# Optimization experiments

Hardware: AMD Instinct MI355X
Metric: run time of the kernel (lower is better)

## Reference

```python
import jax, jax.numpy as jnp
import numpy as np

B, T = 256, 64          # batch, rollout length
D, S, A, E, H = 1024, 64, 32, 1024, 1024  # deter, stoch, action, obs_embed, hidden


def setup_inputs() -> dict:
    key = jax.random.key(0)
    ks = jax.random.split(key, 12)
    f32 = jnp.float32

    def w(k, shape, fan_in):
        return (jax.random.normal(k, shape, f32) / np.float32(np.sqrt(fan_in)))

    return dict(
        obs_embeds=jax.random.normal(ks[0], (B, T, E), f32),
        action_embs=jax.random.normal(ks[1], (B, T, A), f32),
        noise_prior=jax.random.normal(ks[2], (T - 1, B, S), f32),  # randn_like in prior
        noise_post=jax.random.normal(ks[3], (T - 1, B, S), f32),   # randn_like in posterior
        # fc_state_action_embed: Linear(S+A -> D)
        W_sa=w(ks[4], (D, S + A), S + A), b_sa=jnp.zeros((D,), f32),
        # GRUCell(D, D): torch layout [3D, D] with gate order r, z, n
        W_ih=w(ks[5], (3 * D, D), D), b_ih=jnp.zeros((3 * D,), f32),
        W_hh=w(ks[6], (3 * D, D), D), b_hh=jnp.zeros((3 * D,), f32),
        # state_prior: Linear(D->H), ELU, Linear(H->2S)
        Wp1=w(ks[7], (H, D), D), bp1=jnp.zeros((H,), f32),
        Wp2=w(ks[8], (2 * S, H), H), bp2=jnp.zeros((2 * S,), f32),
        # state_posterior: Linear(D+E->H), ELU, Linear(H->2S)
        Wq1=w(ks[9], (H, D + E), D + E), bq1=jnp.zeros((H,), f32),
        Wq2=w(ks[10], (2 * S, H), H), bq2=jnp.zeros((2 * S,), f32),
    )


def reference(obs_embeds, action_embs, noise_prior, noise_post,
              W_sa, b_sa, W_ih, b_ih, W_hh, b_hh,
              Wp1, bp1, Wp2, bp2, Wq1, bq1, Wq2, bq2):
    # observe_rollout: init state is zeros; step t uses obs[:, t+1], action[:, t].
    b = obs_embeds.shape[0]
    h0 = jnp.zeros((b, D), obs_embeds.dtype)
    s0 = jnp.zeros((b, S), obs_embeds.dtype)
    obs_seq = jnp.swapaxes(obs_embeds[:, 1:], 0, 1)   # [T-1, B, E]
    act_seq = jnp.swapaxes(action_embs[:, :-1], 0, 1)  # [T-1, B, A]

    def step(carry, xs):
        h, s = carry  # posterior deter / stoch state from previous step
        obs, act, ep, eq = xs
        # prior: embed (stoch, action) -> GRU update
        e = jax.nn.elu(jnp.concatenate([s, act], -1) @ W_sa.T + b_sa)
        gi = e @ W_ih.T + b_ih
        gh = h @ W_hh.T + b_hh
        ir, iz, ia = jnp.split(gi, 3, axis=-1)
        hr, hz, ha = jnp.split(gh, 3, axis=-1)
        r = jax.nn.sigmoid(ir + hr)
        z = jax.nn.sigmoid(iz + hz)
        n = jnp.tanh(ia + r * ha)
        h_new = (1.0 - z) * n + z * h  # prior deter state
        # prior dist + reparam sample
        pm = jax.nn.elu(h_new @ Wp1.T + bp1) @ Wp2.T + bp2
        pmean, pstd = jnp.split(pm, 2, axis=-1)
        pstd = jax.nn.softplus(pstd) + 0.1
        pstoch = pmean + pstd * ep
        # posterior dist + reparam sample (conditioned on h_new and obs)
        qm = jax.nn.elu(jnp.concatenate([h_new, obs], -1) @ Wq1.T + bq1) @ Wq2.T + bq2
        qmean, qstd = jnp.split(qm, 2, axis=-1)
        qstd = jax.nn.softplus(qstd) + 0.1
        qstoch = qmean + qstd * eq
        out = jnp.concatenate([h_new, pmean, pstd, pstoch, qmean, qstd, qstoch], -1)
        return (h_new, qstoch), out

    _, outs = jax.lax.scan(step, (h0, s0), (obs_seq, act_seq, noise_prior, noise_post))
    # outs: [T-1, B, D + 6S] = (prior deter, prior mean/std/stoch, post mean/std/stoch)
    return outs
```

## Files before the change

kernel.cpp:

```cpp
#include <hip/hip_runtime.h>

typedef __attribute__((ext_vector_type(8))) short short8;
typedef __attribute__((ext_vector_type(4))) float f32x4;

#define OSTEP (256*1408)

#define OFF_WIH  ((size_t)0)
#define OFF_WHH  ((size_t)3145728)
#define OFF_WP1  ((size_t)6291456)
#define OFF_WQ1  ((size_t)7340032)
#define OFF_WP2  ((size_t)9437184)
#define OFF_WQ2  ((size_t)9568256)
#define OFF_HBF0 ((size_t)9699328)
#define OFF_HBF1 ((size_t)9961472)
#define OFF_EBF  ((size_t)10223616)
#define OFF_P1E  ((size_t)10485760)
#define OFF_Q1E  ((size_t)10747904)
#define F32_BYTE_OFF ((size_t)22020096)

__device__ __forceinline__ unsigned short f2bf(float f){
  union { float f; unsigned u; } v; v.f = f;
  unsigned u = v.u;
  u += 0x7fffu + ((u >> 16) & 1u);
  return (unsigned short)(u >> 16);
}
__device__ __forceinline__ float sigf(float x){ return 1.0f/(1.0f+__expf(-x)); }
__device__ __forceinline__ float tanhf_(float x){
  float e = __expf(-2.0f*fabsf(x));
  float t = (1.0f-e)/(1.0f+e);
  return x>=0.f ? t : -t;
}
__device__ __forceinline__ float eluf(float x){ return x>0.f ? x : __expf(x)-1.0f; }
__device__ __forceinline__ float softplusf(float x){ return x>20.f ? x : log1pf(__expf(x)); }
__device__ __forceinline__ short8 ld8(const unsigned short* p){ return *(const short8*)p; }

__global__ void k_prep(const float* __restrict__ wih, const float* __restrict__ whh,
                       const float* __restrict__ wp1, const float* __restrict__ wq1,
                       const float* __restrict__ wp2, const float* __restrict__ wq2,
                       unsigned short* __restrict__ dst){
  size_t i4 = ((size_t)blockIdx.x*256 + threadIdx.x)*4;
  const size_t total = 9699328;
  if(i4 >= total) return;
  const float* src; size_t off;
  if(i4 < 3145728){ src=wih; off=0; }
  else if(i4 < 6291456){ src=whh; off=3145728; }
  else if(i4 < 7340032){ src=wp1; off=6291456; }
  else if(i4 < 9437184){ src=wq1; off=7340032; }
  else if(i4 < 9568256){ src=wp2; off=9437184; }
  else { src=wq2; off=9568256; }
  size_t j = i4 - off;
  float4 v = *(const float4*)(src + j);
  unsigned long long p = (unsigned long long)f2bf(v.x)
                       | ((unsigned long long)f2bf(v.y) << 16)
                       | ((unsigned long long)f2bf(v.z) << 32)
                       | ((unsigned long long)f2bf(v.w) << 48);
  *(unsigned long long*)(dst + i4) = p;
}

__global__ __launch_bounds__(384) void k_gru(
    const unsigned short* __restrict__ e_bf,
    const unsigned short* __restrict__ h_bf,
    const unsigned short* __restrict__ wih_bf,
    const unsigned short* __restrict__ whh_bf,
    const float* __restrict__ b_ih, const float* __restrict__ b_hh,
    const float* __restrict__ hprev, int hprev_ld,
    float* __restrict__ out_t,
    unsigned short* __restrict__ hnext_bf)
{
  int bx = blockIdx.x, by = blockIdx.y;
  int tid = threadIdx.x, w = tid >> 6, lane = tid & 63;
  int g = w % 3; bool isI = (w < 3);
  const unsigned short* A  = isI ? e_bf  : h_bf;
  const unsigned short* Bw = isI ? wih_bf : whh_bf;
  int brow = g*1024 + bx*32;
  int arow = by*32;
  int l15 = lane & 15, q8 = (lane >> 4)*8;

  f32x4 z4 = {0.f,0.f,0.f,0.f};
  f32x4 acc00=z4, acc01=z4, acc10=z4, acc11=z4;

  const unsigned short* pa0 = A  + (size_t)(arow + l15)*1024 + q8;
  const unsigned short* pa1 = pa0 + 16*1024;
  const unsigned short* pb0 = Bw + (size_t)(brow + l15)*1024 + q8;
  const unsigned short* pb1 = pb0 + 16*1024;

  #pragma unroll 4
  for(int kk=0; kk<1024; kk+=32){
    short8 a0 = ld8(pa0+kk), a1 = ld8(pa1+kk);
    short8 b0 = ld8(pb0+kk), b1 = ld8(pb1+kk);
    acc00 = __builtin_amdgcn_mfma_f32_16x16x32_bf16(a0,b0,acc00,0,0,0);
    acc01 = __builtin_amdgcn_mfma_f32_16x16x32_bf16(a0,b1,acc01,0,0,0);
    acc10 = __builtin_amdgcn_mfma_f32_16x16x32_bf16(a1,b0,acc10,0,0,0);
    acc11 = __builtin_amdgcn_mfma_f32_16x16x32_bf16(a1,b1,acc11,0,0,0);
  }

  __shared__ float sg[6][32][33];
  int rr = (lane>>4)*4;
  #pragma unroll
  for(int v=0; v<4; v++){
    sg[w][0 +rr+v][0 +l15] = acc00[v];
    sg[w][0 +rr+v][16+l15] = acc01[v];
    sg[w][16+rr+v][0 +l15] = acc10[v];
    sg[w][16+rr+v][16+l15] = acc11[v];
  }
  __syncthreads();

  for(int i=tid; i<1024; i+=384){
    int m = i>>5, n = i&31;
    int d = bx*32+n, b = by*32+m;
    float ir = sg[0][m][n] + b_ih[d];
    float iz = sg[1][m][n] + b_ih[1024+d];
    float ia = sg[2][m][n] + b_ih[2048+d];
    float hr = sg[3][m][n] + b_hh[d];
    float hz = sg[4][m][n] + b_hh[1024+d];
    float ha = sg[5][m][n] + b_hh[2048+d];
    float r = sigf(ir+hr), zz = sigf(iz+hz);
    float nn = tanhf_(ia + r*ha);
    float hold = hprev[(size_t)b*hprev_ld + d];
    float hnew = (1.f-zz)*nn + zz*hold;
    out_t[(size_t)b*1408 + d] = hnew;
    hnext_bf[(size_t)b*1024 + d] = f2bf(hnew);
  }
}

__global__ __launch_bounds__(256) void k_heads1(
    const unsigned short* __restrict__ hnew_bf,
    const float* __restrict__ obs, int tcol,
    const unsigned short* __restrict__ wp1_bf,
    const unsigned short* __restrict__ wq1_bf,
    const float* __restrict__ bp1, const float* __restrict__ bq1,
    unsigned short* __restrict__ p1e, unsigned short* __restrict__ q1e)
{
  int bx = blockIdx.x, by = blockIdx.y;
  bool isQ = (bx >= 32); int nt = bx & 31;
  int tid = threadIdx.x, w = tid>>6, lane = tid&63;
  int mi = w & 1, ni = w >> 1;
  int l15 = lane & 15, q8 = (lane>>4)*8;
  int arowg = by*32 + mi*16 + l15;
  int browg = nt*32 + ni*16 + l15;

  f32x4 acc = {0.f,0.f,0.f,0.f};
  const unsigned short* pa = hnew_bf + (size_t)arowg*1024 + q8;

  if(!isQ){
    const unsigned short* pb = wp1_bf + (size_t)browg*1024 + q8;
    #pragma unroll 4
    for(int kk=0; kk<1024; kk+=32){
      acc = __builtin_amdgcn_mfma_f32_16x16x32_bf16(ld8(pa+kk), ld8(pb+kk), acc,0,0,0);
    }
  } else {
    const unsigned short* pb = wq1_bf + (size_t)browg*2048 + q8;
    #pragma unroll 4
    for(int kk=0; kk<1024; kk+=32){
      acc = __builtin_amdgcn_mfma_f32_16x16x32_bf16(ld8(pa+kk), ld8(pb+kk), acc,0,0,0);
    }
    const float* obsrow = obs + ((size_t)arowg*64 + tcol)*1024 + q8;
    #pragma unroll 4
    for(int kk=0; kk<1024; kk+=32){
      const float4* f = (const float4*)(obsrow + kk);
      float4 x0 = f[0], x1 = f[1];
      short8 a;
      a[0]=(short)f2bf(x0.x); a[1]=(short)f2bf(x0.y); a[2]=(short)f2bf(x0.z); a[3]=(short)f2bf(x0.w);
      a[4]=(short)f2bf(x1.x); a[5]=(short)f2bf(x1.y); a[6]=(short)f2bf(x1.z); a[7]=(short)f2bf(x1.w);
      acc = __builtin_amdgcn_mfma_f32_16x16x32_bf16(a, ld8(pb+1024+kk), acc,0,0,0);
    }
  }

  const float* bias = isQ ? bq1 : bp1;
  unsigned short* dst = isQ ? q1e : p1e;
  int col = browg;
  float bv = bias[col];
  #pragma unroll
  for(int v=0; v<4; v++){
    int b = by*32 + mi*16 + (lane>>4)*4 + v;
    float val = eluf(acc[v] + bv);
    dst[(size_t)b*1024 + col] = f2bf(val);
  }
}

__global__ __launch_bounds__(256) void k_heads2(
    const unsigned short* __restrict__ p1e, const unsigned short* __restrict__ q1e,
    const unsigned short* __restrict__ wp2_bf, const unsigned short* __restrict__ wq2_bf,
    const float* __restrict__ bp2, const float* __restrict__ bq2,
    float* __restrict__ pm, float* __restrict__ qm)
{
  int bx = blockIdx.x, by = blockIdx.y;
  int col0 = bx*32; bool isQ = (col0 >= 128); int c0 = col0 & 127;
  int tid = threadIdx.x, w = tid>>6, lane = tid&63;
  int mi = w & 1, ni = w >> 1;
  int l15 = lane & 15, q8 = (lane>>4)*8;
  const unsigned short* A  = isQ ? q1e : p1e;
  const unsigned short* Bw = isQ ? wq2_bf : wp2_bf;
  const float* bias = isQ ? bq2 : bp2;
  float* outb = isQ ? qm : pm;

  int arowg = by*32 + mi*16 + l15;
  int browg = c0 + ni*16 + l15;
  f32x4 acc = {0.f,0.f,0.f,0.f};
  const unsigned short* pa = A  + (size_t)arowg*1024 + q8;
  const unsigned short* pb = Bw + (size_t)browg*1024 + q8;
  #pragma unroll 4
  for(int kk=0; kk<1024; kk+=32){
    acc = __builtin_amdgcn_mfma_f32_16x16x32_bf16(ld8(pa+kk), ld8(pb+kk), acc,0,0,0);
  }
  float bv = bias[browg];
  #pragma unroll
  for(int v=0; v<4; v++){
    int b = by*32 + mi*16 + (lane>>4)*4 + v;
    outb[(size_t)b*128 + browg] = acc[v] + bv;
  }
}

__global__ __launch_bounds__(256) void k_sample_e(
    int t_out, int t_act,
    const float* __restrict__ pm, const float* __restrict__ qm,
    const float* __restrict__ noise_p, const float* __restrict__ noise_q,
    const float* __restrict__ act, const float* __restrict__ w_sa,
    const float* __restrict__ b_sa,
    float* __restrict__ out, unsigned short* __restrict__ e_bf)
{
  __shared__ float qst[32*64];
  __shared__ float sact[32*32];
  int bx = blockIdx.x, by = blockIdx.y, tid = threadIdx.x;

  if(t_out >= 0){
    float* out_t = out + (size_t)t_out*OSTEP;
    for(int i=tid; i<2048; i+=256){
      int m = i>>6, s = i&63; int b = by*32+m;
      float qmean = qm[(size_t)b*128 + s];
      float qstd  = softplusf(qm[(size_t)b*128 + 64 + s]) + 0.1f;
      float qs = qmean + qstd * noise_q[((size_t)t_out*256 + b)*64 + s];
      qst[m*64+s] = qs;
      if(bx == 0){
        float pmean = pm[(size_t)b*128 + s];
        float pstd  = softplusf(pm[(size_t)b*128 + 64 + s]) + 0.1f;
        float ps = pmean + pstd * noise_p[((size_t)t_out*256 + b)*64 + s];
        float* o = out_t + (size_t)b*1408;
        o[1024+s] = pmean; o[1088+s] = pstd; o[1152+s] = ps;
        o[1216+s] = qmean; o[1280+s] = qstd; o[1344+s] = qs;
      }
    }
  } else {
    for(int i=tid; i<2048; i+=256) qst[i] = 0.f;
  }
  for(int i=tid; i<1024; i+=256){
    int m = i>>5, k = i&31;
    sact[i] = act[((size_t)(by*32+m)*64 + t_act)*32 + k];
  }
  __syncthreads();

  int n = tid & 31, mb = tid >> 5;
  int d = bx*32 + n;
  const float* wrow = w_sa + (size_t)d*96;
  float a0=b_sa[d], a1=a0, a2=a0, a3=a0;
  for(int k=0; k<64; k++){
    float wv = wrow[k];
    a0 += qst[(mb+ 0)*64+k]*wv;
    a1 += qst[(mb+ 8)*64+k]*wv;
    a2 += qst[(mb+16)*64+k]*wv;
    a3 += qst[(mb+24)*64+k]*wv;
  }
  for(int k=0; k<32; k++){
    float wv = wrow[64+k];
    a0 += sact[(mb+ 0)*32+k]*wv;
    a1 += sact[(mb+ 8)*32+k]*wv;
    a2 += sact[(mb+16)*32+k]*wv;
    a3 += sact[(mb+24)*32+k]*wv;
  }
  e_bf[(size_t)(by*32+mb+ 0)*1024 + d] = f2bf(eluf(a0));
  e_bf[(size_t)(by*32+mb+ 8)*1024 + d] = f2bf(eluf(a1));
  e_bf[(size_t)(by*32+mb+16)*1024 + d] = f2bf(eluf(a2));
  e_bf[(size_t)(by*32+mb+24)*1024 + d] = f2bf(eluf(a3));
}

extern "C" void kernel_launch(void* const* d_in, const int* in_sizes, int n_in,
                              void* d_out, int out_size, void* d_ws, size_t ws_size,
                              hipStream_t stream) {
  const float* obs = (const float*)d_in[0];
  const float* act = (const float*)d_in[1];
  const float* np_ = (const float*)d_in[2];
  const float* nq_ = (const float*)d_in[3];
  const float* wsa = (const float*)d_in[4];
  const float* bsa = (const float*)d_in[5];
  const float* wih = (const float*)d_in[6];
  const float* bih = (const float*)d_in[7];
  const float* whh = (const float*)d_in[8];
  const float* bhh = (const float*)d_in[9];
  const float* wp1 = (const float*)d_in[10];
  const float* bp1 = (const float*)d_in[11];
  const float* wp2 = (const float*)d_in[12];
  const float* bp2 = (const float*)d_in[13];
  const float* wq1 = (const float*)d_in[14];
  const float* bq1 = (const float*)d_in[15];
  const float* wq2 = (const float*)d_in[16];
  const float* bq2 = (const float*)d_in[17];
  float* out = (float*)d_out;

  unsigned short* wsb = (unsigned short*)d_ws;
  unsigned short* wihb = wsb + OFF_WIH;
  unsigned short* whhb = wsb + OFF_WHH;
  unsigned short* wp1b = wsb + OFF_WP1;
  unsigned short* wq1b = wsb + OFF_WQ1;
  unsigned short* wp2b = wsb + OFF_WP2;
  unsigned short* wq2b = wsb + OFF_WQ2;
  unsigned short* hbf0 = wsb + OFF_HBF0;
  unsigned short* hbf1 = wsb + OFF_HBF1;
  unsigned short* ebf  = wsb + OFF_EBF;
  unsigned short* p1e  = wsb + OFF_P1E;
  unsigned short* q1e  = wsb + OFF_Q1E;
  float* f32b = (float*)((char*)d_ws + F32_BYTE_OFF);
  float* h0 = f32b;
  float* pm = f32b + 262144;
  float* qm = f32b + 262144 + 32768;

  hipMemsetAsync(hbf0, 0, 262144*2, stream);
  hipMemsetAsync(h0, 0, 262144*4, stream);

  k_prep<<<9472, 256, 0, stream>>>(wih, whh, wp1, wq1, wp2, wq2, wsb);

  k_sample_e<<<dim3(32,8), 256, 0, stream>>>(-1, 0, pm, qm, np_, nq_, act, wsa, bsa, out, ebf);

  for(int t=0; t<63; t++){
    const unsigned short* hb = (t&1) ? hbf1 : hbf0;
    unsigned short* hbn      = (t&1) ? hbf0 : hbf1;
    const float* hprev = t ? (out + (size_t)(t-1)*OSTEP) : h0;
    int hld = t ? 1408 : 1024;
    k_gru<<<dim3(32,8), 384, 0, stream>>>(ebf, hb, wihb, whhb, bih, bhh,
                                          hprev, hld, out + (size_t)t*OSTEP, hbn);
    k_heads1<<<dim3(64,8), 256, 0, stream>>>(hbn, obs, t+1, wp1b, wq1b, bp1, bq1, p1e, q1e);
    k_heads2<<<dim3(8,8), 256, 0, stream>>>(p1e, q1e, wp2b, wq2b, bp2, bq2, pm, qm);
    k_sample_e<<<dim3(32,8), 256, 0, stream>>>(t, t+1, pm, qm, np_, nq_, act, wsa, bsa, out, ebf);
  }
}
```

Measured before the change: 5.976 ms.

## Halve batch tile per block and split-K head GEMMs to raise parallelism

The GRU kernel now handles 16 batch rows per block instead of 32, doubling the grid to 512 blocks. The two head kernels likewise use 16-row tiles, and their four waves are split across two K halves, reduced through shared memory before bias and activation. The goal is to fill more of the MI355X compute units in these small per-step GEMMs, which run under a long serial chain of launches. The cost is that each weight tile is read by twice as many blocks, adding L2 traffic, plus an extra LDS reduction and barrier in the head kernels.

```diff
diff --git a/kernel.cpp b/kernel.cpp
--- a/kernel.cpp
+++ b/kernel.cpp
@@ -2,6 +2,7 @@
 
 typedef __attribute__((ext_vector_type(8))) short short8;
 typedef __attribute__((ext_vector_type(4))) float f32x4;
+typedef unsigned short us;
 
 #define OSTEP (256*1408)
 
@@ -32,12 +33,12 @@
 }
 __device__ __forceinline__ float eluf(float x){ return x>0.f ? x : __expf(x)-1.0f; }
 __device__ __forceinline__ float softplusf(float x){ return x>20.f ? x : log1pf(__expf(x)); }
-__device__ __forceinline__ short8 ld8(const unsigned short* p){ return *(const short8*)p; }
+__device__ __forceinline__ short8 ld8(const us* p){ return *(const short8*)p; }
 
 __global__ void k_prep(const float* __restrict__ wih, const float* __restrict__ whh,
                        const float* __restrict__ wp1, const float* __restrict__ wq1,
                        const float* __restrict__ wp2, const float* __restrict__ wq2,
-                       unsigned short* __restrict__ dst){
+                       us* __restrict__ dst){
   size_t i4 = ((size_t)blockIdx.x*256 + threadIdx.x)*4;
   const size_t total = 9699328;
   if(i4 >= total) return;
@@ -58,56 +59,48 @@
 }
 
 __global__ __launch_bounds__(384) void k_gru(
-    const unsigned short* __restrict__ e_bf,
-    const unsigned short* __restrict__ h_bf,
-    const unsigned short* __restrict__ wih_bf,
-    const unsigned short* __restrict__ whh_bf,
+    const us* __restrict__ e_bf, const us* __restrict__ h_bf,
+    const us* __restrict__ wih_bf, const us* __restrict__ whh_bf,
     const float* __restrict__ b_ih, const float* __restrict__ b_hh,
     const float* __restrict__ hprev, int hprev_ld,
-    float* __restrict__ out_t,
-    unsigned short* __restrict__ hnext_bf)
+    float* __restrict__ out_t, us* __restrict__ hnext_bf)
 {
   int bx = blockIdx.x, by = blockIdx.y;
   int tid = threadIdx.x, w = tid >> 6, lane = tid & 63;
   int g = w % 3; bool isI = (w < 3);
-  const unsigned short* A  = isI ? e_bf  : h_bf;
-  const unsigned short* Bw = isI ? wih_bf : whh_bf;
+  const us* A  = isI ? e_bf  : h_bf;
+  const us* Bw = isI ? wih_bf : whh_bf;
   int brow = g*1024 + bx*32;
-  int arow = by*32;
+  int arow = by*16;
   int l15 = lane & 15, q8 = (lane >> 4)*8;
 
   f32x4 z4 = {0.f,0.f,0.f,0.f};
-  f32x4 acc00=z4, acc01=z4, acc10=z4, acc11=z4;
-
-  const unsigned short* pa0 = A  + (size_t)(arow + l15)*1024 + q8;
-  const unsigned short* pa1 = pa0 + 16*1024;
-  const unsigned short* pb0 = Bw + (size_t)(brow + l15)*1024 + q8;
-  const unsigned short* pb1 = pb0 + 16*1024;
-
-  #pragma unroll 4
+  f32x4 acc0=z4, acc1=z4;
+
+  const us* pa0 = A  + (size_t)(arow + l15)*1024 + q8;
+  const us* pb0 = Bw + (size_t)(brow + l15)*1024 + q8;
+  const us* pb1 = pb0 + 16*1024;
+
+  #pragma unroll 8
   for(int kk=0; kk<1024; kk+=32){
-    short8 a0 = ld8(pa0+kk), a1 = ld8(pa1+kk);
+    short8 a0 = ld8(pa0+kk);
     short8 b0 = ld8(pb0+kk), b1 = ld8(pb1+kk);
-    acc00 = __builtin_amdgcn_mfma_f32_16x16x32_bf16(a0,b0,acc00,0,0,0);
-    acc01 = __builtin_amdgcn_mfma_f32_16x16x32_bf16(a0,b1,acc01,0,0,0);
-    acc10 = __builtin_amdgcn_mfma_f32_16x16x32_bf16(a1,b0,acc10,0,0,0);
-    acc11 = __builtin_amdgcn_mfma_f32_16x16x32_bf16(a1,b1,acc11,0,0,0);
-  }
-
-  __shared__ float sg[6][32][33];
+    acc0 = __builtin_amdgcn_mfma_f32_16x16x32_bf16(a0,b0,acc0,0,0,0);
+    acc1 = __builtin_amdgcn_mfma_f32_16x16x32_bf16(a0,b1,acc1,0,0,0);
+  }
+
+  __shared__ float sg[6][16][33];
   int rr = (lane>>4)*4;
   #pragma unroll
   for(int v=0; v<4; v++){
-    sg[w][0 +rr+v][0 +l15] = acc00[v];
-    sg[w][0 +rr+v][16+l15] = acc01[v];
-    sg[w][16+rr+v][0 +l15] = acc10[v];
-    sg[w][16+rr+v][16+l15] = acc11[v];
+    sg[w][rr+v][0 +l15] = acc0[v];
+    sg[w][rr+v][16+l15] = acc1[v];
   }
   __syncthreads();
 
-  for(int i=tid; i<1024; i+=384){
+  for(int i=tid; i<512; i+=384){
     int m = i>>5, n = i&31;
-    int d = bx*32+n, b = by*32+m;
+    int d = bx*32+n, b = by*16+m;
     float ir = sg[0][m][n] + b_ih[d];
     float iz = sg[1][m][n] + b_ih[1024+d];
     float ia = sg[2][m][n] + b_ih[2048+d];
@@ -124,90 +117,107 @@
 }
 
 __global__ __launch_bounds__(256) void k_heads1(
-    const unsigned short* __restrict__ hnew_bf,
+    const us* __restrict__ hnew_bf,
     const float* __restrict__ obs, int tcol,
-    const unsigned short* __restrict__ wp1_bf,
-    const unsigned short* __restrict__ wq1_bf,
+    const us* __restrict__ wp1_bf, const us* __restrict__ wq1_bf,
     const float* __restrict__ bp1, const float* __restrict__ bq1,
-    unsigned short* __restrict__ p1e, unsigned short* __restrict__ q1e)
+    us* __restrict__ p1e, us* __restrict__ q1e)
 {
   int bx = blockIdx.x, by = blockIdx.y;
   bool isQ = (bx >= 32); int nt = bx & 31;
   int tid = threadIdx.x, w = tid>>6, lane = tid&63;
-  int mi = w & 1, ni = w >> 1;
+  int ni = w & 1, kh = w >> 1;
   int l15 = lane & 15, q8 = (lane>>4)*8;
-  int arowg = by*32 + mi*16 + l15;
+  int arowg = by*16 + l15;
   int browg = nt*32 + ni*16 + l15;
+  int k0 = kh*512;
 
   f32x4 acc = {0.f,0.f,0.f,0.f};
-  const unsigned short* pa = hnew_bf + (size_t)arowg*1024 + q8;
+  const us* pa = hnew_bf + (size_t)arowg*1024 + q8 + k0;
 
   if(!isQ){
-    const unsigned short* pb = wp1_bf + (size_t)browg*1024 + q8;
-    #pragma unroll 4
-    for(int kk=0; kk<1024; kk+=32){
+    const us* pb = wp1_bf + (size_t)browg*1024 + q8 + k0;
+    #pragma unroll 8
+    for(int kk=0; kk<512; kk+=32){
       acc = __builtin_amdgcn_mfma_f32_16x16x32_bf16(ld8(pa+kk), ld8(pb+kk), acc,0,0,0);
     }
   } else {
-    const unsigned short* pb = wq1_bf + (size_t)browg*2048 + q8;
-    #pragma unroll 4
-    for(int kk=0; kk<1024; kk+=32){
+    const us* pb = wq1_bf + (size_t)browg*2048 + q8 + k0;
+    #pragma unroll 8
+    for(int kk=0; kk<512; kk+=32){
       acc = __builtin_amdgcn_mfma_f32_16x16x32_bf16(ld8(pa+kk), ld8(pb+kk), acc,0,0,0);
     }
-    const float* obsrow = obs + ((size_t)arowg*64 + tcol)*1024 + q8;
+    const float* obsrow = obs + ((size_t)arowg*64 + tcol)*1024 + q8 + k0;
+    const us* pb2 = wq1_bf + (size_t)browg*2048 + 1024 + q8 + k0;
     #pragma unroll 4
-    for(int kk=0; kk<1024; kk+=32){
+    for(int kk=0; kk<512; kk+=32){
       const float4* f = (const float4*)(obsrow + kk);
       float4 x0 = f[0], x1 = f[1];
       short8 a;
       a[0]=(short)f2bf(x0.x); a[1]=(short)f2bf(x0.y); a[2]=(short)f2bf(x0.z); a[3]=(short)f2bf(x0.w);
       a[4]=(short)f2bf(x1.x); a[5]=(short)f2bf(x1.y); a[6]=(short)f2bf(x1.z); a[7]=(short)f2bf(x1.w);
-      acc = __builtin_amdgcn_mfma_f32_16x16x32_bf16(a, ld8(pb+1024+kk), acc,0,0,0);
+      acc = __builtin_amdgcn_mfma_f32_16x16x32_bf16(a, ld8(pb2+kk), acc,0,0,0);
     }
   }
 
+  __shared__ float sg[4][16][17];
+  int rr=(lane>>4)*4;
+  #pragma unroll
+  for(int v=0;v<4;v++) sg[w][rr+v][l15] = acc[v];
+  __syncthreads();
+
   const float* bias = isQ ? bq1 : bp1;
-  unsigned short* dst = isQ ? q1e : p1e;
-  int col = browg;
-  float bv = bias[col];
-  #pragma unroll
-  for(int v=0; v<4; v++){
-    int b = by*32 + mi*16 + (lane>>4)*4 + v;
-    float val = eluf(acc[v] + bv);
-    dst[(size_t)b*1024 + col] = f2bf(val);
+  us* dst = isQ ? q1e : p1e;
+  for(int i=tid; i<512; i+=256){
+    int m = i>>5, n = i&31;
+    int nni = n>>4, nn = n&15;
+    float val = sg[nni][m][nn] + sg[2+nni][m][nn];
+    int col = nt*32 + n;
+    int b = by*16 + m;
+    dst[(size_t)b*1024 + col] = f2bf(eluf(val + bias[col]));
   }
 }
 
 __global__ __launch_bounds__(256) void k_heads2(
-    const unsigned short* __restrict__ p1e, const unsigned short* __restrict__ q1e,
-    const unsigned short* __restrict__ wp2_bf, const unsigned short* __restrict__ wq2_bf,
+    const us* __restrict__ p1e, const us* __restrict__ q1e,
+    const us* __restrict__ wp2_bf, const us* __restrict__ wq2_bf,
     const float* __restrict__ bp2, const float* __restrict__ bq2,
     float* __restrict__ pm, float* __restrict__ qm)
 {
   int bx = blockIdx.x, by = blockIdx.y;
   int col0 = bx*32; bool isQ = (col0 >= 128); int c0 = col0 & 127;
   int tid = threadIdx.x, w = tid>>6, lane = tid&63;
-  int mi = w & 1, ni = w >> 1;
+  int ni = w & 1, kh = w >> 1;
   int l15 = lane & 15, q8 = (lane>>4)*8;
-  const unsigned short* A  = isQ ? q1e : p1e;
-  const unsigned short* Bw = isQ ? wq2_bf : wp2_bf;
+  const us* A  = isQ ? q1e : p1e;
+  const us* Bw = isQ ? wq2_bf : wp2_bf;
   const float* bias = isQ ? bq2 : bp2;
   float* outb = isQ ? qm : pm;
 
-  int arowg = by*32 + mi*16 + l15;
+  int arowg = by*16 + l15;
   int browg = c0 + ni*16 + l15;
+  int k0 = kh*512;
   f32x4 acc = {0.f,0.f,0.f,0.f};
-  const unsigned short* pa = A  + (size_t)arowg*1024 + q8;
-  const unsigned short* pb = Bw + (size_t)browg*1024 + q8;
-  #pragma unroll 4
-  for(int kk=0; kk<1024; kk+=32){
+  const us* pa = A  + (size_t)arowg*1024 + q8 + k0;
+  const us* pb = Bw + (size_t)browg*1024 + q8 + k0;
+  #pragma unroll 8
+  for(int kk=0; kk<512; kk+=32){
     acc = __builtin_amdgcn_mfma_f32_16x16x32_bf16(ld8(pa+kk), ld8(pb+kk), acc,0,0,0);
   }
-  float bv = bias[browg];
+
+  __shared__ float sg[4][16][17];
+  int rr=(lane>>4)*4;
   #pragma unroll
-  for(int v=0; v<4; v++){
-    int b = by*32 + mi*16 + (lane>>4)*4 + v;
-    outb[(size_t)b*128 + browg] = acc[v] + bv;
+  for(int v=0;v<4;v++) sg[w][rr+v][l15] = acc[v];
+  __syncthreads();
+
+  for(int i=tid; i<512; i+=256){
+    int m = i>>5, n = i&31;
+    int nni = n>>4, nn = n&15;
+    float val = sg[nni][m][nn] + sg[2+nni][m][nn];
+    int col = c0 + n;
+    int b = by*16 + m;
+    outb[(size_t)b*128 + col] = val + bias[col];
   }
 }
 
@@ -217,7 +227,7 @@
     const float* __restrict__ noise_p, const float* __restrict__ noise_q,
     const float* __restrict__ act, const float* __restrict__ w_sa,
     const float* __restrict__ b_sa,
-    float* __restrict__ out, unsigned short* __restrict__ e_bf)
+    float* __restrict__ out, us* __restrict__ e_bf)
 {
   __shared__ float qst[32*64];
   __shared__ float sact[32*32];
@@ -295,19 +305,19 @@
   const float* wq2 = (const float*)d_in[16];
   const float* bq2 = (const float*)d_in[17];
   float* out = (float*)d_out;
-
-  unsigned short* wsb = (unsigned short*)d_ws;
-  unsigned short* wihb = wsb + OFF_WIH;
-  unsigned short* whhb = wsb + OFF_WHH;
-  unsigned short* wp1b = wsb + OFF_WP1;
-  unsigned short* wq1b = wsb + OFF_WQ1;
-  unsigned short* wp2b = wsb + OFF_WP2;
-  unsigned short* wq2b = wsb + OFF_WQ2;
-  unsigned short* hbf0 = wsb + OFF_HBF0;
-  unsigned short* hbf1 = wsb + OFF_HBF1;
-  unsigned short* ebf  = wsb + OFF_EBF;
-  unsigned short* p1e  = wsb + OFF_P1E;
-  unsigned short* q1e  = wsb + OFF_Q1E;
+  us* wsb = (us*)d_ws;
+
+  us* wihb = wsb + OFF_WIH;
+  us* whhb = wsb + OFF_WHH;
+  us* wp1b = wsb + OFF_WP1;
+  us* wq1b = wsb + OFF_WQ1;
+  us* wp2b = wsb + OFF_WP2;
+  us* wq2b = wsb + OFF_WQ2;
+  us* hbf0 = wsb + OFF_HBF0;
+  us* hbf1 = wsb + OFF_HBF1;
+  us* ebf  = wsb + OFF_EBF;
+  us* p1e  = wsb + OFF_P1E;
+  us* q1e  = wsb + OFF_Q1E;
   float* f32b = (float*)((char*)d_ws + F32_BYTE_OFF);
   float* h0 = f32b;
   float* pm = f32b + 262144;
@@ -321,14 +331,14 @@
   k_sample_e<<<dim3(32,8), 256, 0, stream>>>(-1, 0, pm, qm, np_, nq_, act, wsa, bsa, out, ebf);
 
   for(int t=0; t<63; t++){
-    const unsigned short* hb = (t&1) ? hbf1 : hbf0;
-    unsigned short* hbn      = (t&1) ? hbf0 : hbf1;
+    const us* hb = (t&1) ? hbf1 : hbf0;
+    us* hbn      = (t&1) ? hbf0 : hbf1;
     const float* hprev = t ? (out + (size_t)(t-1)*OSTEP) : h0;
     int hld = t ? 1408 : 1024;
-    k_gru<<<dim3(32,8), 384, 0, stream>>>(ebf, hb, wihb, whhb, bih, bhh,
-                                          hprev, hld, out + (size_t)t*OSTEP, hbn);
-    k_heads1<<<dim3(64,8), 256, 0, stream>>>(hbn, obs, t+1, wp1b, wq1b, bp1, bq1, p1e, q1e);
-    k_heads2<<<dim3(8,8), 256, 0, stream>>>(p1e, q1e, wp2b, wq2b, bp2, bq2, pm, qm);
+    k_gru<<<dim3(32,16), 384, 0, stream>>>(ebf, hb, wihb, whhb, bih, bhh,
+                                           hprev, hld, out + (size_t)t*OSTEP, hbn);
+    k_heads1<<<dim3(64,16), 256, 0, stream>>>(hbn, obs, t+1, wp1b, wq1b, bp1, bq1, p1e, q1e);
+    k_heads2<<<dim3(8,16), 256, 0, stream>>>(p1e, q1e, wp2b, wq2b, bp2, bq2, pm, qm);
     k_sample_e<<<dim3(32,8), 256, 0, stream>>>(t, t+1, pm, qm, np_, nq_, act, wsa, bsa, out, ebf);
   }
 }
```

Result: slower. 6.226 ms (+4.2%).

## Fuse second head layer into sampling kernel and stage obs in LDS

Applied to the files above, without the earlier changes.

Merges the head output GEMM into the sampling/embedding kernel so pm/qm stay in shared memory, cutting one launch and a global round-trip per step. Each block now recomputes the full 256-wide head output for its rows, which is redundant across column blocks, and the grid shrinks to 64 blocks with more work per thread. The posterior head kernel also converts the obs rows to bf16 once into LDS instead of per warp.

```diff
diff --git a/kernel.cpp b/kernel.cpp
--- a/kernel.cpp
+++ b/kernel.cpp
@@ -2,6 +2,7 @@
 
 typedef __attribute__((ext_vector_type(8))) short short8;
 typedef __attribute__((ext_vector_type(4))) float f32x4;
+typedef unsigned short us;
 
 #define OSTEP (256*1408)
 
@@ -32,12 +33,12 @@
 }
 __device__ __forceinline__ float eluf(float x){ return x>0.f ? x : __expf(x)-1.0f; }
 __device__ __forceinline__ float softplusf(float x){ return x>20.f ? x : log1pf(__expf(x)); }
-__device__ __forceinline__ short8 ld8(const unsigned short* p){ return *(const short8*)p; }
+__device__ __forceinline__ short8 ld8(const us* p){ return *(const short8*)p; }
 
 __global__ void k_prep(const float* __restrict__ wih, const float* __restrict__ whh,
                        const float* __restrict__ wp1, const float* __restrict__ wq1,
                        const float* __restrict__ wp2, const float* __restrict__ wq2,
-                       unsigned short* __restrict__ dst){
+                       us* __restrict__ dst){
   size_t i4 = ((size_t)blockIdx.x*256 + threadIdx.x)*4;
   const size_t total = 9699328;
   if(i4 >= total) return;
@@ -58,20 +59,17 @@
 }
 
 __global__ __launch_bounds__(384) void k_gru(
-    const unsigned short* __restrict__ e_bf,
-    const unsigned short* __restrict__ h_bf,
-    const unsigned short* __restrict__ wih_bf,
-    const unsigned short* __restrict__ whh_bf,
+    const us* __restrict__ e_bf, const us* __restrict__ h_bf,
+    const us* __restrict__ wih_bf, const us* __restrict__ whh_bf,
     const float* __restrict__ b_ih, const float* __restrict__ b_hh,
     const float* __restrict__ hprev, int hprev_ld,
-    float* __restrict__ out_t,
-    unsigned short* __restrict__ hnext_bf)
+    float* __restrict__ out_t, us* __restrict__ hnext_bf)
 {
   int bx = blockIdx.x, by = blockIdx.y;
   int tid = threadIdx.x, w = tid >> 6, lane = tid & 63;
   int g = w % 3; bool isI = (w < 3);
-  const unsigned short* A  = isI ? e_bf  : h_bf;
-  const unsigned short* Bw = isI ? wih_bf : whh_bf;
+  const us* A  = isI ? e_bf  : h_bf;
+  const us* Bw = isI ? wih_bf : whh_bf;
   int brow = g*1024 + bx*32;
   int arow = by*32;
   int l15 = lane & 15, q8 = (lane >> 4)*8;
@@ -79,10 +77,10 @@
   f32x4 z4 = {0.f,0.f,0.f,0.f};
   f32x4 acc00=z4, acc01=z4, acc10=z4, acc11=z4;
 
-  const unsigned short* pa0 = A  + (size_t)(arow + l15)*1024 + q8;
-  const unsigned short* pa1 = pa0 + 16*1024;
-  const unsigned short* pb0 = Bw + (size_t)(brow + l15)*1024 + q8;
-  const unsigned short* pb1 = pb0 + 16*1024;
+  const us* pa0 = A  + (size_t)(arow + l15)*1024 + q8;
+  const us* pa1 = pa0 + 16*1024;
+  const us* pb0 = Bw + (size_t)(brow + l15)*1024 + q8;
+  const us* pb1 = pb0 + 16*1024;
 
   #pragma unroll 4
   for(int kk=0; kk<1024; kk+=32){
@@ -124,13 +122,13 @@
 }
 
 __global__ __launch_bounds__(256) void k_heads1(
-    const unsigned short* __restrict__ hnew_bf,
+    const us* __restrict__ hnew_bf,
     const float* __restrict__ obs, int tcol,
-    const unsigned short* __restrict__ wp1_bf,
-    const unsigned short* __restrict__ wq1_bf,
+    const us* __restrict__ wp1_bf, const us* __restrict__ wq1_bf,
     const float* __restrict__ bp1, const float* __restrict__ bq1,
-    unsigned short* __restrict__ p1e, unsigned short* __restrict__ q1e)
+    us* __restrict__ p1e, us* __restrict__ q1e)
 {
+  __shared__ us sobs[32][1032];
   int bx = blockIdx.x, by = blockIdx.y;
   bool isQ = (bx >= 32); int nt = bx & 31;
   int tid = threadIdx.x, w = tid>>6, lane = tid&63;
@@ -140,34 +138,42 @@
   int browg = nt*32 + ni*16 + l15;
 
   f32x4 acc = {0.f,0.f,0.f,0.f};
-  const unsigned short* pa = hnew_bf + (size_t)arowg*1024 + q8;
+  const us* pa = hnew_bf + (size_t)arowg*1024 + q8;
 
   if(!isQ){
-    const unsigned short* pb = wp1_bf + (size_t)browg*1024 + q8;
+    const us* pb = wp1_bf + (size_t)browg*1024 + q8;
     #pragma unroll 4
     for(int kk=0; kk<1024; kk+=32){
       acc = __builtin_amdgcn_mfma_f32_16x16x32_bf16(ld8(pa+kk), ld8(pb+kk), acc,0,0,0);
     }
   } else {
-    const unsigned short* pb = wq1_bf + (size_t)browg*2048 + q8;
+    for(int i=tid; i<32*256; i+=256){
+      int r = i>>8, c4 = (i&255)*4;
+      const float4* f = (const float4*)(obs + ((size_t)(by*32+r)*64 + tcol)*1024 + c4);
+      float4 x = *f;
+      unsigned long long p = (unsigned long long)f2bf(x.x)
+                           | ((unsigned long long)f2bf(x.y) << 16)
+                           | ((unsigned long long)f2bf(x.z) << 32)
+                           | ((unsigned long long)f2bf(x.w) << 48);
+      *(unsigned long long*)(&sobs[r][c4]) = p;
+    }
+    __syncthreads();
+
+    const us* pb = wq1_bf + (size_t)browg*2048 + q8;
     #pragma unroll 4
     for(int kk=0; kk<1024; kk+=32){
       acc = __builtin_amdgcn_mfma_f32_16x16x32_bf16(ld8(pa+kk), ld8(pb+kk), acc,0,0,0);
     }
-    const float* obsrow = obs + ((size_t)arowg*64 + tcol)*1024 + q8;
+    const us* po = &sobs[mi*16 + l15][q8];
+    const us* pb2 = wq1_bf + (size_t)browg*2048 + 1024 + q8;
     #pragma unroll 4
     for(int kk=0; kk<1024; kk+=32){
-      const float4* f = (const float4*)(obsrow + kk);
-      float4 x0 = f[0], x1 = f[1];
-      short8 a;
-      a[0]=(short)f2bf(x0.x); a[1]=(short)f2bf(x0.y); a[2]=(short)f2bf(x0.z); a[3]=(short)f2bf(x0.w);
-      a[4]=(short)f2bf(x1.x); a[5]=(short)f2bf(x1.y); a[6]=(short)f2bf(x1.z); a[7]=(short)f2bf(x1.w);
-      acc = __builtin_amdgcn_mfma_f32_16x16x32_bf16(a, ld8(pb+1024+kk), acc,0,0,0);
+      acc = __builtin_amdgcn_mfma_f32_16x16x32_bf16(ld8(po+kk), ld8(pb2+kk), acc,0,0,0);
     }
   }
 
   const float* bias = isQ ? bq1 : bp1;
-  unsigned short* dst = isQ ? q1e : p1e;
+  us* dst = isQ ? q1e : p1e;
   int col = browg;
   float bv = bias[col];
   #pragma unroll
@@ -178,62 +184,55 @@
   }
 }
 
-__global__ __launch_bounds__(256) void k_heads2(
-    const unsigned short* __restrict__ p1e, const unsigned short* __restrict__ q1e,
-    const unsigned short* __restrict__ wp2_bf, const unsigned short* __restrict__ wq2_bf,
+__global__ __launch_bounds__(256) void k_tail(
+    int t_out, int t_act,
+    const us* __restrict__ p1e, const us* __restrict__ q1e,
+    const us* __restrict__ wp2_bf, const us* __restrict__ wq2_bf,
     const float* __restrict__ bp2, const float* __restrict__ bq2,
-    float* __restrict__ pm, float* __restrict__ qm)
-{
-  int bx = blockIdx.x, by = blockIdx.y;
-  int col0 = bx*32; bool isQ = (col0 >= 128); int c0 = col0 & 127;
-  int tid = threadIdx.x, w = tid>>6, lane = tid&63;
-  int mi = w & 1, ni = w >> 1;
-  int l15 = lane & 15, q8 = (lane>>4)*8;
-  const unsigned short* A  = isQ ? q1e : p1e;
-  const unsigned short* Bw = isQ ? wq2_bf : wp2_bf;
-  const float* bias = isQ ? bq2 : bp2;
-  float* outb = isQ ? qm : pm;
-
-  int arowg = by*32 + mi*16 + l15;
-  int browg = c0 + ni*16 + l15;
-  f32x4 acc = {0.f,0.f,0.f,0.f};
-  const unsigned short* pa = A  + (size_t)arowg*1024 + q8;
-  const unsigned short* pb = Bw + (size_t)browg*1024 + q8;
-  #pragma unroll 4
-  for(int kk=0; kk<1024; kk+=32){
-    acc = __builtin_amdgcn_mfma_f32_16x16x32_bf16(ld8(pa+kk), ld8(pb+kk), acc,0,0,0);
-  }
-  float bv = bias[browg];
-  #pragma unroll
-  for(int v=0; v<4; v++){
-    int b = by*32 + mi*16 + (lane>>4)*4 + v;
-    outb[(size_t)b*128 + browg] = acc[v] + bv;
-  }
-}
-
-__global__ __launch_bounds__(256) void k_sample_e(
-    int t_out, int t_act,
-    const float* __restrict__ pm, const float* __restrict__ qm,
     const float* __restrict__ noise_p, const float* __restrict__ noise_q,
     const float* __restrict__ act, const float* __restrict__ w_sa,
     const float* __restrict__ b_sa,
-    float* __restrict__ out, unsigned short* __restrict__ e_bf)
+    float* __restrict__ out, us* __restrict__ e_bf)
 {
+  __shared__ float pmq[32][258];
   __shared__ float qst[32*64];
   __shared__ float sact[32*32];
   int bx = blockIdx.x, by = blockIdx.y, tid = threadIdx.x;
+  int w = tid>>6, lane = tid&63;
+  int l15 = lane&15, q8 = (lane>>4)*8;
+
+  if(t_out >= 0){
+    int mi = w&1, cg = w>>1;
+    const us* A  = cg ? q1e : p1e;
+    const us* Bw = cg ? wq2_bf : wp2_bf;
+    int arowg = by*32 + mi*16 + l15;
+    const us* pa = A + (size_t)arowg*1024 + q8;
+    for(int ct=0; ct<8; ct++){
+      const us* pb = Bw + (size_t)(ct*16 + l15)*1024 + q8;
+      f32x4 acc = {0.f,0.f,0.f,0.f};
+      #pragma unroll 4
+      for(int kk=0; kk<1024; kk+=32){
+        acc = __builtin_amdgcn_mfma_f32_16x16x32_bf16(ld8(pa+kk), ld8(pb+kk), acc,0,0,0);
+      }
+      int rr = (lane>>4)*4;
+      #pragma unroll
+      for(int v=0; v<4; v++)
+        pmq[mi*16 + rr + v][cg*128 + ct*16 + l15] = acc[v];
+    }
+  }
+  __syncthreads();
 
   if(t_out >= 0){
     float* out_t = out + (size_t)t_out*OSTEP;
     for(int i=tid; i<2048; i+=256){
       int m = i>>6, s = i&63; int b = by*32+m;
-      float qmean = qm[(size_t)b*128 + s];
-      float qstd  = softplusf(qm[(size_t)b*128 + 64 + s]) + 0.1f;
+      float qmean = pmq[m][128+s] + bq2[s];
+      float qstd  = softplusf(pmq[m][192+s] + bq2[64+s]) + 0.1f;
       float qs = qmean + qstd * noise_q[((size_t)t_out*256 + b)*64 + s];
       qst[m*64+s] = qs;
       if(bx == 0){
-        float pmean = pm[(size_t)b*128 + s];
-        float pstd  = softplusf(pm[(size_t)b*128 + 64 + s]) + 0.1f;
+        float pmean = pmq[m][s] + bp2[s];
+        float pstd  = softplusf(pmq[m][64+s] + bp2[64+s]) + 0.1f;
         float ps = pmean + pstd * noise_p[((size_t)t_out*256 + b)*64 + s];
         float* o = out_t + (size_t)b*1408;
         o[1024+s] = pmean; o[1088+s] = pstd; o[1152+s] = ps;
@@ -249,28 +248,28 @@
   }
   __syncthreads();
 
-  int n = tid & 31, mb = tid >> 5;
-  int d = bx*32 + n;
-  const float* wrow = w_sa + (size_t)d*96;
-  float a0=b_sa[d], a1=a0, a2=a0, a3=a0;
-  for(int k=0; k<64; k++){
-    float wv = wrow[k];
-    a0 += qst[(mb+ 0)*64+k]*wv;
-    a1 += qst[(mb+ 8)*64+k]*wv;
-    a2 += qst[(mb+16)*64+k]*wv;
-    a3 += qst[(mb+24)*64+k]*wv;
-  }
-  for(int k=0; k<32; k++){
-    float wv = wrow[64+k];
-    a0 += sact[(mb+ 0)*32+k]*wv;
-    a1 += sact[(mb+ 8)*32+k]*wv;
-    a2 += sact[(mb+16)*32+k]*wv;
-    a3 += sact[(mb+24)*32+k]*wv;
-  }
-  e_bf[(size_t)(by*32+mb+ 0)*1024 + d] = f2bf(eluf(a0));
-  e_bf[(size_t)(by*32+mb+ 8)*1024 + d] = f2bf(eluf(a1));
-  e_bf[(size_t)(by*32+mb+16)*1024 + d] = f2bf(eluf(a2));
-  e_bf[(size_t)(by*32+mb+24)*1024 + d] = f2bf(eluf(a3));
+  int c2 = (lane)*2, mb0 = w*8;
+  for(int cc=0; cc<2; cc++){
+    int d = bx*128 + c2 + cc;
+    const float* wrow = w_sa + (size_t)d*96;
+    float a[8];
+    float bias = b_sa[d];
+    #pragma unroll
+    for(int j=0;j<8;j++) a[j] = bias;
+    for(int k=0; k<64; k++){
+      float wv = wrow[k];
+      #pragma unroll
+      for(int j=0;j<8;j++) a[j] += qst[(mb0+j)*64+k]*wv;
+    }
+    for(int k=0; k<32; k++){
+      float wv = wrow[64+k];
+      #pragma unroll
+      for(int j=0;j<8;j++) a[j] += sact[(mb0+j)*32+k]*wv;
+    }
+    #pragma unroll
+    for(int j=0;j<8;j++)
+      e_bf[(size_t)(by*32+mb0+j)*1024 + d] = f2bf(eluf(a[j]));
+  }
 }
 
 extern "C" void kernel_launch(void* const* d_in, const int* in_sizes, int n_in,
@@ -295,40 +294,39 @@
   const float* wq2 = (const float*)d_in[16];
   const float* bq2 = (const float*)d_in[17];
   float* out = (float*)d_out;
-
-  unsigned short* wsb = (unsigned short*)d_ws;
-  unsigned short* wihb = wsb + OFF_WIH;
-  unsigned short* whhb = wsb + OFF_WHH;
-  unsigned short* wp1b = wsb + OFF_WP1;
-  unsigned short* wq1b = wsb + OFF_WQ1;
-  unsigned short* wp2b = wsb + OFF_WP2;
-  unsigned short* wq2b = wsb + OFF_WQ2;
-  unsigned short* hbf0 = wsb + OFF_HBF0;
-  unsigned short* hbf1 = wsb + OFF_HBF1;
-  unsigned short* ebf  = wsb + OFF_EBF;
-  unsigned short* p1e  = wsb + OFF_P1E;
-  unsigned short* q1e  = wsb + OFF_Q1E;
+  us* wsb = (us*)d_ws;
+
+  us* wihb = wsb + OFF_WIH;
+  us* whhb = wsb + OFF_WHH;
+  us* wp1b = wsb + OFF_WP1;
+  us* wq1b = wsb + OFF_WQ1;
+  us* wp2b = wsb + OFF_WP2;
+  us* wq2b = wsb + OFF_WQ2;
+  us* hbf0 = wsb + OFF_HBF0;
+  us* hbf1 = wsb + OFF_HBF1;
+  us* ebf  = wsb + OFF_EBF;
+  us* p1e  = wsb + OFF_P1E;
+  us* q1e  = wsb + OFF_Q1E;
   float* f32b = (float*)((char*)d_ws + F32_BYTE_OFF);
   float* h0 = f32b;
-  float* pm = f32b + 262144;
-  float* qm = f32b + 262144 + 32768;
 
   hipMemsetAsync(hbf0, 0, 262144*2, stream);
   hipMemsetAsync(h0, 0, 262144*4, stream);
 
   k_prep<<<9472, 256, 0, stream>>>(wih, whh, wp1, wq1, wp2, wq2, wsb);
 
-  k_sample_e<<<dim3(32,8), 256, 0, stream>>>(-1, 0, pm, qm, np_, nq_, act, wsa, bsa, out, ebf);
+  k_tail<<<dim3(8,8), 256, 0, stream>>>(-1, 0, p1e, q1e, wp2b, wq2b, bp2, bq2,
+                                        np_, nq_, act, wsa, bsa, out, ebf);
 
   for(int t=0; t<63; t++){
-    const unsigned short* hb = (t&1) ? hbf1 : hbf0;
-    unsigned short* hbn      = (t&1) ? hbf0 : hbf1;
+    const us* hb = (t&1) ? hbf1 : hbf0;
+    us* hbn      = (t&1) ? hbf0 : hbf1;
     const float* hprev = t ? (out + (size_t)(t-1)*OSTEP) : h0;
     int hld = t ? 1408 : 1024;
     k_gru<<<dim3(32,8), 384, 0, stream>>>(ebf, hb, wihb, whhb, bih, bhh,
                                           hprev, hld, out + (size_t)t*OSTEP, hbn);
     k_heads1<<<dim3(64,8), 256, 0, stream>>>(hbn, obs, t+1, wp1b, wq1b, bp1, bq1, p1e, q1e);
-    k_heads2<<<dim3(8,8), 256, 0, stream>>>(p1e, q1e, wp2b, wq2b, bp2, bq2, pm, qm);
-    k_sample_e<<<dim3(32,8), 256, 0, stream>>>(t, t+1, pm, qm, np_, nq_, act, wsa, bsa, out, ebf);
-  }
-}
+    k_tail<<<dim3(8,8), 256, 0, stream>>>(t, t+1, p1e, q1e, wp2b, wq2b, bp2, bq2,
+                                          np_, nq_, act, wsa, bsa, out, ebf);
+  }
+}
```

Result: slower. 9.870 ms (+65.1%).
